# Kernel optimization log

Hardware: AMD Instinct MI355X
Metric: run time of the kernel (lower is better)

The kernel has to match this reference:

```python
import jax, jax.numpy as jnp
import numpy as np

WAYS, SHOTS = 5, 5
F_DIM, HID = 1024, 512          # num_node_feats, int(1024*0.5)
BATCH = 2048                    # num_tasks
N = WAYS * SHOTS + 1            # 26 samples per episode
BN_EPS = 1e-5


def setup_inputs() -> dict:
    key = jax.random.key(0)
    ks = jax.random.split(key, 12)
    d = {"node_feats": jax.random.normal(ks[0], (BATCH, N, F_DIM), jnp.float32)}
    # conv1 (1x1): F_DIM -> HID, bn1; conv2: HID -> HID, bn2; conv4: HID -> F_DIM
    d["w1"] = jax.random.normal(ks[1], (HID, F_DIM), jnp.float32) * (1.0 / np.sqrt(F_DIM))
    d["b1"] = jax.random.normal(ks[2], (HID,), jnp.float32) * 0.01
    d["g1"] = jnp.ones((HID,), jnp.float32)
    d["be1"] = jnp.zeros((HID,), jnp.float32)
    d["m1"] = jax.random.normal(ks[3], (HID,), jnp.float32) * 0.1
    d["v1"] = jax.random.uniform(ks[4], (HID,), jnp.float32, 0.5, 1.5)
    d["w2"] = jax.random.normal(ks[5], (HID, HID), jnp.float32) * (1.0 / np.sqrt(HID))
    d["b2"] = jax.random.normal(ks[6], (HID,), jnp.float32) * 0.01
    d["g2"] = jnp.ones((HID,), jnp.float32)
    d["be2"] = jnp.zeros((HID,), jnp.float32)
    d["m2"] = jax.random.normal(ks[7], (HID,), jnp.float32) * 0.1
    d["v2"] = jax.random.uniform(ks[8], (HID,), jnp.float32, 0.5, 1.5)
    d["w3"] = jax.random.normal(ks[9], (F_DIM, HID), jnp.float32) * (1.0 / np.sqrt(HID))
    d["b3"] = jax.random.normal(ks[10], (F_DIM,), jnp.float32) * 0.01
    return d


def _conv1x1(x, w, b):
    # x: [B, Cin, N], w: [Cout, Cin] -> [B, Cout, N]
    return jnp.einsum('bcn,oc->bon', x, w) + b[None, :, None]


def _bn(x, g, be, m, v):
    # inference BatchNorm1d over channel dim of [B, C, N]
    scale = g / jnp.sqrt(v + BN_EPS)
    return (x - m[None, :, None]) * scale[None, :, None] + be[None, :, None]


def _forward(node_feats, w1, b1, g1, be1, m1, v1, w2, b2, g2, be2, m2, v2, w3, b3):
    B, n, F = node_feats.shape  # n == WAYS*SHOTS+1
    # in-place per-class mean on the transpose view also mutates node_feats in torch:
    sup = node_feats[:, :WAYS * SHOTS].reshape(B, WAYS, SHOTS, F)
    sup = jnp.broadcast_to(sup.mean(axis=2, keepdims=True), sup.shape).reshape(B, WAYS * SHOTS, F)
    nf = jnp.concatenate([sup, node_feats[:, WAYS * SHOTS:]], axis=1)  # [B, N, F]

    x = nf.transpose(0, 2, 1)  # [B, F, N]
    x = jax.nn.leaky_relu(_bn(_conv1x1(x, w1, b1), g1, be1, m1, v1), 0.01)
    x = jax.nn.leaky_relu(_bn(_conv1x1(x, w2, b2), g2, be2, m2, v2), 0.01)
    att = jax.nn.sigmoid(_conv1x1(x, w3, b3))  # [B, F, N]

    # sim_cal: cosine sim of u_ij = a_i*a_j*x_i vs v_ij = a_i*a_j*x_j, fused into matmuls.
    a = att.transpose(0, 2, 1)       # [B, N, F]
    a2 = a * a                       # attention squared
    P = a2 * nf                      # dot(u,v)   = (P P^T)[i,j]
    Q = a2 * nf * nf                 # ||u_ij||^2 = (Q a2^T)[i,j]
    dots = jnp.einsum('bif,bjf->bij', P, P)    # [B, N, N]
    n2 = jnp.einsum('bif,bjf->bij', Q, a2)     # [B, N, N]
    nrm = jnp.sqrt(n2)
    sim = dots / (nrm * nrm.transpose(0, 2, 1))
    pred = jnp.stack([sim, 1.0 - sim], axis=1)  # [B, 2, N, N]
    return jnp.clip(pred, 0.0, 1.0)


def reference(node_feats, w1, b1, g1, be1, m1, v1, w2, b2, g2, be2, m2, v2, w3, b3):
    return _forward(node_feats, w1, b1, g1, be1, m1, v1, w2, b2, g2, be2, m2, v2, w3, b3)
```

## Files before the change

kernel.cpp:

```cpp
#include <hip/hip_runtime.h>
#include <hip/hip_bf16.h>
#include <math.h>

typedef __bf16 bf16_t;
typedef bf16_t bf16x8 __attribute__((ext_vector_type(8)));
typedef float f32x4 __attribute__((ext_vector_type(4)));

#define WAYS 5
#define SHOTS 5
#define F_DIM 1024
#define HID 512
#define BATCH 2048
#define NN 26
#define NC 6
#define MROWS (BATCH * NC)

__global__ __launch_bounds__(256)
void cvt_kernel(const float* __restrict__ in, bf16_t* __restrict__ out, int n) {
    int i = (blockIdx.x * 256 + threadIdx.x) * 4;
    if (i < n) {
        float4 v = *(const float4*)(in + i);
        out[i + 0] = (bf16_t)v.x;
        out[i + 1] = (bf16_t)v.y;
        out[i + 2] = (bf16_t)v.z;
        out[i + 3] = (bf16_t)v.w;
    }
}

__global__ __launch_bounds__(128)
void nfc_kernel(const float* __restrict__ node, float* __restrict__ nfc_f,
                bf16_t* __restrict__ nfc_b) {
    int row = blockIdx.x;
    int b = row / NC;
    int w = row - b * NC;
    int f = threadIdx.x * 8;
    const float* src = node + (size_t)b * NN * F_DIM;
    float acc[8];
    if (w < WAYS) {
        #pragma unroll
        for (int e = 0; e < 8; ++e) acc[e] = 0.f;
        #pragma unroll
        for (int s = 0; s < SHOTS; ++s) {
            const float* r = src + (size_t)(w * SHOTS + s) * F_DIM + f;
            float4 v0 = *(const float4*)r;
            float4 v1 = *(const float4*)(r + 4);
            acc[0] += v0.x; acc[1] += v0.y; acc[2] += v0.z; acc[3] += v0.w;
            acc[4] += v1.x; acc[5] += v1.y; acc[6] += v1.z; acc[7] += v1.w;
        }
        #pragma unroll
        for (int e = 0; e < 8; ++e) acc[e] *= 0.2f;
    } else {
        const float* r = src + (size_t)25 * F_DIM + f;
        float4 v0 = *(const float4*)r;
        float4 v1 = *(const float4*)(r + 4);
        acc[0] = v0.x; acc[1] = v0.y; acc[2] = v0.z; acc[3] = v0.w;
        acc[4] = v1.x; acc[5] = v1.y; acc[6] = v1.z; acc[7] = v1.w;
    }
    float* df = nfc_f + (size_t)row * F_DIM + f;
    *(float4*)df       = make_float4(acc[0], acc[1], acc[2], acc[3]);
    *(float4*)(df + 4) = make_float4(acc[4], acc[5], acc[6], acc[7]);
    bf16x8 ob;
    #pragma unroll
    for (int e = 0; e < 8; ++e) ob[e] = (bf16_t)acc[e];
    *(bf16x8*)(nfc_b + (size_t)row * F_DIM + f) = ob;
}

template<int EPI, typename OutT>
__global__ __launch_bounds__(256)
void gemm_bt(const bf16_t* __restrict__ A, const bf16_t* __restrict__ W,
             OutT* __restrict__ C, int M, int N, int K,
             const float* __restrict__ bias, const float* __restrict__ gam,
             const float* __restrict__ bet, const float* __restrict__ mu,
             const float* __restrict__ var) {
    __shared__ bf16_t As[128 * 32];
    __shared__ bf16_t Bs[128 * 32];
    const int tid = threadIdx.x;
    const int lane = tid & 63, wid = tid >> 6;
    const int bm = blockIdx.y * 128, bn = blockIdx.x * 128;
    const int l15 = lane & 15, quad = lane >> 4;
    const int wm = (wid & 1) * 64, wn = (wid >> 1) * 64;

    const int srow = wid * 32;
    const int lrow = lane >> 2;
    const int lcol = (lane & 3) * 8;
    const bf16_t* gA = A + (size_t)(bm + srow + lrow) * K + lcol;
    const bf16_t* gB = W + (size_t)(bn + srow + lrow) * K + lcol;
    bf16_t* lA = &As[srow * 32];
    bf16_t* lB = &Bs[srow * 32];

    f32x4 acc[4][4] = {};

    for (int k0 = 0; k0 < K; k0 += 32) {
        __syncthreads();
        #pragma unroll
        for (int q = 0; q < 2; ++q) {
            __builtin_amdgcn_global_load_lds(
                (const __attribute__((address_space(1))) void*)(gA + (size_t)q * 16 * K + k0),
                (__attribute__((address_space(3))) void*)(lA + q * 16 * 32), 16, 0, 0);
            __builtin_amdgcn_global_load_lds(
                (const __attribute__((address_space(1))) void*)(gB + (size_t)q * 16 * K + k0),
                (__attribute__((address_space(3))) void*)(lB + q * 16 * 32), 16, 0, 0);
        }
        __syncthreads();
        bf16x8 af[4], bfr[4];
        #pragma unroll
        for (int mi = 0; mi < 4; ++mi)
            af[mi] = *(const bf16x8*)&As[(wm + mi * 16 + l15) * 32 + quad * 8];
        #pragma unroll
        for (int ni = 0; ni < 4; ++ni)
            bfr[ni] = *(const bf16x8*)&Bs[(wn + ni * 16 + l15) * 32 + quad * 8];
        #pragma unroll
        for (int mi = 0; mi < 4; ++mi)
            #pragma unroll
            for (int ni = 0; ni < 4; ++ni)
                acc[mi][ni] = __builtin_amdgcn_mfma_f32_16x16x32_bf16(af[mi], bfr[ni], acc[mi][ni], 0, 0, 0);
    }

    #pragma unroll
    for (int ni = 0; ni < 4; ++ni) {
        const int n = bn + wn + ni * 16 + l15;
        float s, t;
        if constexpr (EPI == 0) {
            float sg = gam[n] * rsqrtf(var[n] + 1e-5f);
            s = sg;
            t = (bias[n] - mu[n]) * sg + bet[n];
        } else {
            s = 1.0f;
            t = bias[n];
        }
        #pragma unroll
        for (int mi = 0; mi < 4; ++mi) {
            const int m = bm + wm + mi * 16 + quad * 4;
            #pragma unroll
            for (int r = 0; r < 4; ++r) {
                float y = acc[mi][ni][r] * s + t;
                if constexpr (EPI == 0) {
                    y = y > 0.0f ? y : 0.01f * y;
                } else {
                    y = 1.0f / (1.0f + __expf(-y));
                }
                C[(size_t)(m + r) * N + n] = (OutT)y;
            }
        }
    }
}

__global__ __launch_bounds__(256)
void sim_kernel(const float* __restrict__ nfc, const float* __restrict__ att,
                float* __restrict__ out) {
    __shared__ float sx[NC * F_DIM];
    __shared__ float sa[NC * F_DIM];
    __shared__ float dmat[NC * NC], n2mat[NC * NC], simc[NC * NC];
    const int b = blockIdx.x, tid = threadIdx.x;
    const float* xs = nfc + (size_t)b * NC * F_DIM;
    const float* as = att + (size_t)b * NC * F_DIM;
    for (int i = tid * 4; i < NC * F_DIM; i += 256 * 4) {
        *(float4*)&sx[i] = *(const float4*)&xs[i];
        *(float4*)&sa[i] = *(const float4*)&as[i];
    }
    __syncthreads();
    const int lane = tid & 63, wid = tid >> 6;
    const int ti[21] = {0,0,0,0,0,0,1,1,1,1,1,2,2,2,2,3,3,3,4,4,5};
    const int tj[21] = {0,1,2,3,4,5,1,2,3,4,5,2,3,4,5,3,4,5,4,5,5};
    for (int t = wid; t < 21; t += 4) {
        const int i = ti[t], j = tj[t];
        float d = 0.f, qij = 0.f, qji = 0.f;
        for (int f = lane; f < F_DIM; f += 64) {
            float ai = sa[i * F_DIM + f], aj = sa[j * F_DIM + f];
            float xi = sx[i * F_DIM + f], xj = sx[j * F_DIM + f];
            float a2i = ai * ai, a2j = aj * aj;
            float pi = a2i * xi, pj = a2j * xj;
            d   += pi * pj;
            qij += pi * xi * a2j;
            qji += pj * xj * a2i;
        }
        #pragma unroll
        for (int off = 32; off > 0; off >>= 1) {
            d   += __shfl_xor(d, off);
            qij += __shfl_xor(qij, off);
            qji += __shfl_xor(qji, off);
        }
        if (lane == 0) {
            dmat[i * NC + j] = d; dmat[j * NC + i] = d;
            n2mat[i * NC + j] = qij; n2mat[j * NC + i] = qji;
        }
    }
    __syncthreads();
    if (tid < NC * NC) {
        int i = tid / NC, j = tid - (tid / NC) * NC;
        simc[tid] = dmat[tid] / sqrtf(n2mat[i * NC + j] * n2mat[j * NC + i]);
    }
    __syncthreads();
    float* o = out + (size_t)b * (2 * NN * NN);
    for (int e = tid; e < 2 * NN * NN; e += 256) {
        int ch = e / (NN * NN);
        int rem = e - ch * (NN * NN);
        int i = rem / NN, j = rem - (rem / NN) * NN;
        float s = simc[(i / 5) * NC + (j / 5)];
        float v = ch ? 1.0f - s : s;
        v = fminf(fmaxf(v, 0.0f), 1.0f);
        o[e] = v;
    }
}

extern "C" void kernel_launch(void* const* d_in, const int* in_sizes, int n_in,
                              void* d_out, int out_size, void* d_ws, size_t ws_size,
                              hipStream_t stream) {
    const float* node = (const float*)d_in[0];
    const float* w1  = (const float*)d_in[1];
    const float* b1  = (const float*)d_in[2];
    const float* g1  = (const float*)d_in[3];
    const float* be1 = (const float*)d_in[4];
    const float* m1  = (const float*)d_in[5];
    const float* v1  = (const float*)d_in[6];
    const float* w2  = (const float*)d_in[7];
    const float* b2  = (const float*)d_in[8];
    const float* g2  = (const float*)d_in[9];
    const float* be2 = (const float*)d_in[10];
    const float* m2  = (const float*)d_in[11];
    const float* v2  = (const float*)d_in[12];
    const float* w3  = (const float*)d_in[13];
    const float* b3  = (const float*)d_in[14];
    float* out = (float*)d_out;

    char* ws = (char*)d_ws;
    size_t off = 0;
    float*  nfc_f = (float*) (ws + off); off += (size_t)MROWS * F_DIM * 4;
    bf16_t* nfc_b = (bf16_t*)(ws + off); off += (size_t)MROWS * F_DIM * 2;
    bf16_t* w1b   = (bf16_t*)(ws + off); off += (size_t)HID * F_DIM * 2;
    bf16_t* w2b   = (bf16_t*)(ws + off); off += (size_t)HID * HID * 2;
    bf16_t* w3b   = (bf16_t*)(ws + off); off += (size_t)F_DIM * HID * 2;
    bf16_t* x1    = (bf16_t*)(ws + off); off += (size_t)MROWS * HID * 2;
    bf16_t* x2    = (bf16_t*)(ws + off); off += (size_t)MROWS * HID * 2;
    float*  attb  = (float*) (ws + off); off += (size_t)MROWS * F_DIM * 4;

    cvt_kernel<<<(HID * F_DIM / 4 + 255) / 256, 256, 0, stream>>>(w1, w1b, HID * F_DIM);
    cvt_kernel<<<(HID * HID / 4 + 255) / 256, 256, 0, stream>>>(w2, w2b, HID * HID);
    cvt_kernel<<<(F_DIM * HID / 4 + 255) / 256, 256, 0, stream>>>(w3, w3b, F_DIM * HID);
    nfc_kernel<<<MROWS, 128, 0, stream>>>(node, nfc_f, nfc_b);
    gemm_bt<0, bf16_t><<<dim3(HID / 128, MROWS / 128), 256, 0, stream>>>(
        nfc_b, w1b, x1, MROWS, HID, F_DIM, b1, g1, be1, m1, v1);
    gemm_bt<0, bf16_t><<<dim3(HID / 128, MROWS / 128), 256, 0, stream>>>(
        x1, w2b, x2, MROWS, HID, HID, b2, g2, be2, m2, v2);
    gemm_bt<1, float><<<dim3(F_DIM / 128, MROWS / 128), 256, 0, stream>>>(
        x2, w3b, attb, MROWS, F_DIM, HID, b3, nullptr, nullptr, nullptr, nullptr);
    sim_kernel<<<BATCH, 256, 0, stream>>>(nfc_f, attb, out);
}
```

Before: 471.7 us.

## Store intermediates in bf16, merge weight casts, and narrow GEMM N-tiles

The fp32 copy of the class-collapsed features is dropped and the attention output is stored as bf16, so the similarity kernel reads bf16 for both and widens to fp32 in shared memory. The three weight conversion launches become one kernel writing a contiguous buffer. The first two GEMMs switch to 64-wide N tiles, doubling their block count for better CU occupancy. This cuts global memory traffic and launch overhead, but computing the cosine similarity from bf16 inputs adds rounding error.

```diff
diff --git a/kernel.cpp b/kernel.cpp
--- a/kernel.cpp
+++ b/kernel.cpp
@@ -15,21 +15,29 @@
 #define NC 6
 #define MROWS (BATCH * NC)
 
+#define S1 (HID * F_DIM)
+#define S2 (HID * HID)
+#define S3 (F_DIM * HID)
+
 __global__ __launch_bounds__(256)
-void cvt_kernel(const float* __restrict__ in, bf16_t* __restrict__ out, int n) {
+void cvt_all_kernel(const float* __restrict__ w1, const float* __restrict__ w2,
+                    const float* __restrict__ w3, bf16_t* __restrict__ out) {
     int i = (blockIdx.x * 256 + threadIdx.x) * 4;
-    if (i < n) {
-        float4 v = *(const float4*)(in + i);
-        out[i + 0] = (bf16_t)v.x;
-        out[i + 1] = (bf16_t)v.y;
-        out[i + 2] = (bf16_t)v.z;
-        out[i + 3] = (bf16_t)v.w;
-    }
+    if (i >= S1 + S2 + S3) return;
+    const float* src;
+    int j = i;
+    if (i < S1)            { src = w1; }
+    else if (i < S1 + S2)  { src = w2; j = i - S1; }
+    else                   { src = w3; j = i - S1 - S2; }
+    float4 v = *(const float4*)(src + j);
+    out[i + 0] = (bf16_t)v.x;
+    out[i + 1] = (bf16_t)v.y;
+    out[i + 2] = (bf16_t)v.z;
+    out[i + 3] = (bf16_t)v.w;
 }
 
 __global__ __launch_bounds__(128)
-void nfc_kernel(const float* __restrict__ node, float* __restrict__ nfc_f,
-                bf16_t* __restrict__ nfc_b) {
+void nfc_kernel(const float* __restrict__ node, bf16_t* __restrict__ nfc_b) {
     int row = blockIdx.x;
     int b = row / NC;
     int w = row - b * NC;
@@ -56,68 +64,68 @@
         acc[0] = v0.x; acc[1] = v0.y; acc[2] = v0.z; acc[3] = v0.w;
         acc[4] = v1.x; acc[5] = v1.y; acc[6] = v1.z; acc[7] = v1.w;
     }
-    float* df = nfc_f + (size_t)row * F_DIM + f;
-    *(float4*)df       = make_float4(acc[0], acc[1], acc[2], acc[3]);
-    *(float4*)(df + 4) = make_float4(acc[4], acc[5], acc[6], acc[7]);
     bf16x8 ob;
     #pragma unroll
     for (int e = 0; e < 8; ++e) ob[e] = (bf16_t)acc[e];
     *(bf16x8*)(nfc_b + (size_t)row * F_DIM + f) = ob;
 }
 
-template<int EPI, typename OutT>
+template<int EPI, int TN>
 __global__ __launch_bounds__(256)
 void gemm_bt(const bf16_t* __restrict__ A, const bf16_t* __restrict__ W,
-             OutT* __restrict__ C, int M, int N, int K,
+             bf16_t* __restrict__ C, int M, int N, int K,
              const float* __restrict__ bias, const float* __restrict__ gam,
              const float* __restrict__ bet, const float* __restrict__ mu,
              const float* __restrict__ var) {
+    constexpr int NI = TN / 32;
     __shared__ bf16_t As[128 * 32];
-    __shared__ bf16_t Bs[128 * 32];
+    __shared__ bf16_t Bs[TN * 32];
     const int tid = threadIdx.x;
     const int lane = tid & 63, wid = tid >> 6;
-    const int bm = blockIdx.y * 128, bn = blockIdx.x * 128;
+    const int bm = blockIdx.y * 128, bn = blockIdx.x * TN;
     const int l15 = lane & 15, quad = lane >> 4;
-    const int wm = (wid & 1) * 64, wn = (wid >> 1) * 64;
-
-    const int srow = wid * 32;
+    const int wm = (wid & 1) * 64, wn = (wid >> 1) * (TN / 2);
+
+    const int srowA = wid * 32;
+    const int srowB = wid * (TN / 4);
     const int lrow = lane >> 2;
     const int lcol = (lane & 3) * 8;
-    const bf16_t* gA = A + (size_t)(bm + srow + lrow) * K + lcol;
-    const bf16_t* gB = W + (size_t)(bn + srow + lrow) * K + lcol;
-    bf16_t* lA = &As[srow * 32];
-    bf16_t* lB = &Bs[srow * 32];
-
-    f32x4 acc[4][4] = {};
+    const bf16_t* gA = A + (size_t)(bm + srowA + lrow) * K + lcol;
+    const bf16_t* gB = W + (size_t)(bn + srowB + lrow) * K + lcol;
+    bf16_t* lA = &As[srowA * 32];
+    bf16_t* lB = &Bs[srowB * 32];
+
+    f32x4 acc[4][NI] = {};
 
     for (int k0 = 0; k0 < K; k0 += 32) {
         __syncthreads();
         #pragma unroll
-        for (int q = 0; q < 2; ++q) {
+        for (int q = 0; q < 2; ++q)
             __builtin_amdgcn_global_load_lds(
                 (const __attribute__((address_space(1))) void*)(gA + (size_t)q * 16 * K + k0),
                 (__attribute__((address_space(3))) void*)(lA + q * 16 * 32), 16, 0, 0);
+        #pragma unroll
+        for (int q = 0; q < TN / 64; ++q)
             __builtin_amdgcn_global_load_lds(
                 (const __attribute__((address_space(1))) void*)(gB + (size_t)q * 16 * K + k0),
                 (__attribute__((address_space(3))) void*)(lB + q * 16 * 32), 16, 0, 0);
-        }
         __syncthreads();
-        bf16x8 af[4], bfr[4];
+        bf16x8 af[4], bfr[NI];
         #pragma unroll
         for (int mi = 0; mi < 4; ++mi)
             af[mi] = *(const bf16x8*)&As[(wm + mi * 16 + l15) * 32 + quad * 8];
         #pragma unroll
-        for (int ni = 0; ni < 4; ++ni)
+        for (int ni = 0; ni < NI; ++ni)
             bfr[ni] = *(const bf16x8*)&Bs[(wn + ni * 16 + l15) * 32 + quad * 8];
         #pragma unroll
         for (int mi = 0; mi < 4; ++mi)
             #pragma unroll
-            for (int ni = 0; ni < 4; ++ni)
+            for (int ni = 0; ni < NI; ++ni)
                 acc[mi][ni] = __builtin_amdgcn_mfma_f32_16x16x32_bf16(af[mi], bfr[ni], acc[mi][ni], 0, 0, 0);
     }
 
     #pragma unroll
-    for (int ni = 0; ni < 4; ++ni) {
+    for (int ni = 0; ni < NI; ++ni) {
         const int n = bn + wn + ni * 16 + l15;
         float s, t;
         if constexpr (EPI == 0) {
@@ -139,24 +147,26 @@
                 } else {
                     y = 1.0f / (1.0f + __expf(-y));
                 }
-                C[(size_t)(m + r) * N + n] = (OutT)y;
+                C[(size_t)(m + r) * N + n] = (bf16_t)y;
             }
         }
     }
 }
 
 __global__ __launch_bounds__(256)
-void sim_kernel(const float* __restrict__ nfc, const float* __restrict__ att,
+void sim_kernel(const bf16_t* __restrict__ nfc, const bf16_t* __restrict__ att,
                 float* __restrict__ out) {
     __shared__ float sx[NC * F_DIM];
     __shared__ float sa[NC * F_DIM];
     __shared__ float dmat[NC * NC], n2mat[NC * NC], simc[NC * NC];
     const int b = blockIdx.x, tid = threadIdx.x;
-    const float* xs = nfc + (size_t)b * NC * F_DIM;
-    const float* as = att + (size_t)b * NC * F_DIM;
-    for (int i = tid * 4; i < NC * F_DIM; i += 256 * 4) {
-        *(float4*)&sx[i] = *(const float4*)&xs[i];
-        *(float4*)&sa[i] = *(const float4*)&as[i];
+    const bf16_t* xs = nfc + (size_t)b * NC * F_DIM;
+    const bf16_t* as = att + (size_t)b * NC * F_DIM;
+    for (int i = tid * 8; i < NC * F_DIM; i += 256 * 8) {
+        bf16x8 vx = *(const bf16x8*)&xs[i];
+        bf16x8 va = *(const bf16x8*)&as[i];
+        #pragma unroll
+        for (int e = 0; e < 8; ++e) { sx[i + e] = (float)vx[e]; sa[i + e] = (float)va[e]; }
     }
     __syncthreads();
     const int lane = tid & 63, wid = tid >> 6;
@@ -225,24 +235,20 @@
 
     char* ws = (char*)d_ws;
     size_t off = 0;
-    float*  nfc_f = (float*) (ws + off); off += (size_t)MROWS * F_DIM * 4;
+    bf16_t* wall  = (bf16_t*)(ws + off); off += (size_t)(S1 + S2 + S3) * 2;
+    bf16_t* w1b = wall, *w2b = wall + S1, *w3b = wall + S1 + S2;
     bf16_t* nfc_b = (bf16_t*)(ws + off); off += (size_t)MROWS * F_DIM * 2;
-    bf16_t* w1b   = (bf16_t*)(ws + off); off += (size_t)HID * F_DIM * 2;
-    bf16_t* w2b   = (bf16_t*)(ws + off); off += (size_t)HID * HID * 2;
-    bf16_t* w3b   = (bf16_t*)(ws + off); off += (size_t)F_DIM * HID * 2;
     bf16_t* x1    = (bf16_t*)(ws + off); off += (size_t)MROWS * HID * 2;
     bf16_t* x2    = (bf16_t*)(ws + off); off += (size_t)MROWS * HID * 2;
-    float*  attb  = (float*) (ws + off); off += (size_t)MROWS * F_DIM * 4;
-
-    cvt_kernel<<<(HID * F_DIM / 4 + 255) / 256, 256, 0, stream>>>(w1, w1b, HID * F_DIM);
-    cvt_kernel<<<(HID * HID / 4 + 255) / 256, 256, 0, stream>>>(w2, w2b, HID * HID);
-    cvt_kernel<<<(F_DIM * HID / 4 + 255) / 256, 256, 0, stream>>>(w3, w3b, F_DIM * HID);
-    nfc_kernel<<<MROWS, 128, 0, stream>>>(node, nfc_f, nfc_b);
-    gemm_bt<0, bf16_t><<<dim3(HID / 128, MROWS / 128), 256, 0, stream>>>(
+    bf16_t* attb  = (bf16_t*)(ws + off); off += (size_t)MROWS * F_DIM * 2;
+
+    cvt_all_kernel<<<((S1 + S2 + S3) / 4 + 255) / 256, 256, 0, stream>>>(w1, w2, w3, wall);
+    nfc_kernel<<<MROWS, 128, 0, stream>>>(node, nfc_b);
+    gemm_bt<0, 64><<<dim3(HID / 64, MROWS / 128), 256, 0, stream>>>(
         nfc_b, w1b, x1, MROWS, HID, F_DIM, b1, g1, be1, m1, v1);
-    gemm_bt<0, bf16_t><<<dim3(HID / 128, MROWS / 128), 256, 0, stream>>>(
+    gemm_bt<0, 64><<<dim3(HID / 64, MROWS / 128), 256, 0, stream>>>(
         x1, w2b, x2, MROWS, HID, HID, b2, g2, be2, m2, v2);
-    gemm_bt<1, float><<<dim3(F_DIM / 128, MROWS / 128), 256, 0, stream>>>(
+    gemm_bt<1, 128><<<dim3(F_DIM / 128, MROWS / 128), 256, 0, stream>>>(
         x2, w3b, attb, MROWS, F_DIM, HID, b3, nullptr, nullptr, nullptr, nullptr);
-    sim_kernel<<<BATCH, 256, 0, stream>>>(nfc_f, attb, out);
-}
+    sim_kernel<<<BATCH, 256, 0, stream>>>(nfc_b, attb, out);
+}
```

Result: faster. 445.5 us (-5.6%).
